# Kernel tuning notes

Hardware: AMD Instinct MI355X
Metric: run time of the kernel (lower is better)

## Reference

```python
import jax, jax.numpy as jnp
import numpy as np

N, NNODES, CIN, COUT = 64, 512, 32, 64


def setup_inputs() -> dict:
    key = jax.random.key(0)
    k1, k2, k3, k4, k5 = jax.random.split(key, 5)
    A = jax.random.normal(k1, (N, NNODES, NNODES), dtype=jnp.float32)
    X = jax.random.normal(k2, (N, NNODES, CIN), dtype=jnp.float32)
    A_coeffs = jax.random.normal(k3, (5 + 2 * CIN,), dtype=jnp.float32)
    x_num = 4 + 2 * CIN
    scale = np.sqrt(2.0) / (COUT + x_num)
    X_coeffs_1 = jax.random.normal(k4, (COUT, x_num), dtype=jnp.float32) * scale
    X_coeffs_2 = jax.random.normal(k5, (COUT, x_num), dtype=jnp.float32) * scale
    return {"A": A, "X": X, "A_coeffs": A_coeffs,
            "X_coeffs_1": X_coeffs_1, "X_coeffs_2": X_coeffs_2}


def _forward(A, X, A_coeffs, W1, W2):
    n = A.shape[-1]
    C = X.shape[-1]
    Xt = jnp.swapaxes(X, -1, -2)                      # N,C,n
    diag = jnp.diagonal(A, axis1=-2, axis2=-1)        # N,n
    mean_diag = diag.mean(-1)                         # N
    mean_cols = A.mean(-1)                            # N,n
    mean_all = mean_cols.mean(-1)                     # N
    mean_X = Xt.mean(-1)                              # N,C

    c = A_coeffs
    w6 = c[5:5 + C]                                   # coeffs for a6 (X_i + X_j)
    w7 = c[5 + C:5 + 2 * C]                           # coeffs for a7 (mean_X)
    # Fold the 'd,ndij->nij' contraction over the 7 basis tensors into
    # scalar/row/col broadcast terms (identical math, no N x (5+2C) x n x n tensor).
    s = jnp.einsum('c,nci->ni', w6, Xt)               # N,n
    const = c[1] * mean_all + c[2] * mean_diag + jnp.einsum('c,nc->n', w7, mean_X)
    vec = c[3] * mean_cols + c[4] * diag + s          # N,n
    A_t = c[0] * A + const[:, None, None] + vec[:, :, None] + vec[:, None, :]

    # X basis out_x: N x (4+2C) x n, order [x1, x2, x3, x4, x5, x6]
    ones_n = jnp.ones((1, 1, n), A.dtype)
    out_x = jnp.concatenate([
        Xt,                                           # x1: N,C,n
        mean_X[:, :, None] * ones_n,                  # x2: N,C,n
        mean_cols[:, None, :],                        # x3: N,1,n
        diag[:, None, :],                             # x4: N,1,n
        mean_diag[:, None, None] * ones_n,            # x5: N,1,n
        mean_all[:, None, None] * ones_n,             # x6: N,1,n
    ], axis=1)
    X1 = jnp.einsum('bd,ndi->nbi', W1, out_x)         # N,B,n
    X2 = jnp.einsum('bd,ndi->nbi', W2, out_x)         # N,B,n
    out = jnp.einsum('nij,nbj->nbi', A_t, X1) / n + X2  # N,B,n
    return jnp.swapaxes(out, -1, -2)                  # N,n,B


def reference(A, X, A_coeffs, X_coeffs_1, X_coeffs_2):
    return _forward(A, X, A_coeffs, X_coeffs_1, X_coeffs_2)
```

## Files before the change

kernel.cpp:

```cpp
#include <hip/hip_runtime.h>
#include <hip/hip_bf16.h>

#define NB 64
#define NN 512
#define CI 32
#define CO 64
#define XN 68
#define YR 80

typedef __attribute__((ext_vector_type(8))) short bf16x8;
typedef __attribute__((ext_vector_type(4))) float f32x4;

__device__ inline short f2bf(float f) {
  union { __hip_bfloat16 h; unsigned short u; } cv;
  cv.h = __float2bfloat16(f);
  return (short)cv.u;
}

__device__ inline bf16x8 cvt8(float4 a, float4 b) {
  bf16x8 r;
  r[0] = f2bf(a.x); r[1] = f2bf(a.y); r[2] = f2bf(a.z); r[3] = f2bf(a.w);
  r[4] = f2bf(b.x); r[5] = f2bf(b.y); r[6] = f2bf(b.z); r[7] = f2bf(b.w);
  return r;
}

__global__ __launch_bounds__(256) void k1x(
    const float* __restrict__ A, const float* __restrict__ X,
    const float* __restrict__ cf, const float* __restrict__ W1,
    float* __restrict__ mc, float* __restrict__ dg, float* __restrict__ vec,
    float* __restrict__ pA, float* __restrict__ pD,
    float* __restrict__ pmX, float* __restrict__ ptC, float* __restrict__ pS,
    unsigned short* __restrict__ Yext) {
  int b = blockIdx.x, ch = blockIdx.y;
  int t = threadIdx.x, w = t >> 6, lane = t & 63;
  int r0 = ch * 16;
  const float* Ab = A + (size_t)b * NN * NN;
  __shared__ float sXc[16][33];
  __shared__ float scf[69];
  __shared__ float sMc[16], sDg[16], sVec[16], wsum[4];

  if (t < 69) scf[t] = cf[t];
  {
    int j = t >> 4, c = (t & 15) * 2;
    float2 xv = *(const float2*)(X + ((size_t)b * NN + r0 + j) * CI + c);
    sXc[j][c] = xv.x; sXc[j][c + 1] = xv.y;
  }
  float4 v0[4], v1[4];
#pragma unroll
  for (int m = 0; m < 4; ++m) {
    const float* rp = Ab + (size_t)(r0 + w * 4 + m) * NN;
    v0[m] = *(const float4*)(rp + lane * 4);
    v1[m] = *(const float4*)(rp + 256 + lane * 4);
  }
  float accR = 0.f;
#pragma unroll
  for (int m = 0; m < 4; ++m) {
    float s = (v0[m].x + v0[m].y) + (v0[m].z + v0[m].w) +
              (v1[m].x + v1[m].y) + (v1[m].z + v1[m].w);
#pragma unroll
    for (int off = 1; off < 64; off <<= 1) s += __shfl_xor(s, off, 64);
    if (lane == 0) {
      float m_ = s * (1.0f / NN);
      mc[b * NN + r0 + w * 4 + m] = m_;
      sMc[w * 4 + m] = m_;
    }
    accR += s;
  }
  if (lane == 0) wsum[w] = accR;
  if (t < 16) {
    float d = Ab[(size_t)(r0 + t) * NN + r0 + t];
    dg[b * NN + r0 + t] = d;
    sDg[t] = d;
  }
  __syncthreads();

  float c0n = scf[0] * (1.0f / NN);

  if (t < 16) {
    float u = 0.f;
#pragma unroll
    for (int c = 0; c < CI; ++c) u += scf[5 + c] * sXc[t][c];
    float vj = scf[3] * sMc[t] + scf[4] * sDg[t] + u;
    vec[b * NN + r0 + t] = vj;
    sVec[t] = vj;
  } else if (t == 16) {
    pA[b * 32 + ch] = wsum[0] + wsum[1] + wsum[2] + wsum[3];
    float sd = 0.f;
#pragma unroll
    for (int k = 0; k < 16; ++k) sd += sDg[k];
    pD[b * 32 + ch] = sd;
  }

  {
    int ra = lane & 15, kg = lane >> 4, g = lane >> 4;
    const float* wp = W1 + (w * 16 + ra) * XN + kg * 8;
    bf16x8 wf = cvt8(*(const float4*)wp, *(const float4*)(wp + 4));
    const float* xp = &sXc[ra][kg * 8];
    bf16x8 xf = cvt8(*(const float4*)xp, *(const float4*)(xp + 4));
    f32x4 zero = {0.f, 0.f, 0.f, 0.f};
    f32x4 d = __builtin_amdgcn_mfma_f32_16x16x32_bf16(xf, wf, zero, 0, 0, 0);
    union { unsigned short u[4]; uint2 v; } pk;
#pragma unroll
    for (int r = 0; r < 4; ++r) pk.u[r] = (unsigned short)f2bf(d[r] * c0n);
    *(uint2*)(Yext + ((size_t)b * YR + w * 16 + ra) * NN + r0 + g * 4) = pk.v;
  }
  if (t < 16) {
    Yext[((size_t)b * YR + 64) * NN + r0 + t] = (unsigned short)f2bf(sMc[t] * c0n);
  } else if (t < 32) {
    Yext[((size_t)b * YR + 65) * NN + r0 + (t - 16)] = (unsigned short)f2bf(sDg[t - 16] * c0n);
  } else if (t < 32 + 224) {
    int u2 = t - 32;
    int row = 66 + (u2 >> 4), col = r0 + (u2 & 15);
    Yext[((size_t)b * YR + row) * NN + col] = 0;
  }
  __syncthreads();

  if (t < 32) {
    float s1 = 0.f, s2 = 0.f;
#pragma unroll
    for (int r = 0; r < 16; ++r) {
      float xv = sXc[r][t];
      s1 += xv;
      s2 += sVec[r] * xv;
    }
    pmX[((size_t)b * 32 + ch) * 32 + t] = s1;
    ptC[((size_t)b * 32 + ch) * 32 + t] = s2;
  } else if (t < 35) {
    float s = 0.f;
    if (t == 32) { for (int r = 0; r < 16; ++r) s += sVec[r]; }
    if (t == 33) { for (int r = 0; r < 16; ++r) s += sVec[r] * sMc[r]; }
    if (t == 34) { for (int r = 0; r < 16; ++r) s += sVec[r] * sDg[r]; }
    pS[((size_t)b * 32 + ch) * 3 + (t - 32)] = s;
  }
}

__global__ __launch_bounds__(256) void kW(
    const float* __restrict__ cf, const float* __restrict__ W1,
    const float* __restrict__ W2, const float* __restrict__ pA,
    const float* __restrict__ pD, const float* __restrict__ pmX,
    const float* __restrict__ ptC, const float* __restrict__ pS,
    float* __restrict__ colv, float* __restrict__ sconst) {
  int gb = blockIdx.x, t = threadIdx.x;
  int bb0 = gb * 4;
  __shared__ float sW1[64][69], sW2[64][69];
  __shared__ float mXs[4][33], tCs[4][33];
  __shared__ float scal[4][6];
  __shared__ float scf[69];
  if (t < 69) scf[t] = cf[t];
  for (int idx = t; idx < 64 * XN; idx += 256) {
    int r = idx / XN, c = idx - r * XN;
    sW1[r][c] = W1[idx];
    sW2[r][c] = W2[idx];
  }
  if (t < 128) {
    int bb = t >> 5, c = t & 31, b = bb0 + bb;
    float s1 = 0.f, s2 = 0.f;
#pragma unroll
    for (int k = 0; k < 32; ++k) {
      s1 += pmX[((size_t)b * 32 + k) * 32 + c];
      s2 += ptC[((size_t)b * 32 + k) * 32 + c];
    }
    mXs[bb][c] = s1 * (1.0f / NN);
    tCs[bb][c] = s2;
  } else if (t < 132) {
    int bb = t - 128, b = bb0 + bb;
    float sA = 0.f, sD = 0.f;
#pragma unroll
    for (int k = 0; k < 32; ++k) { sA += pA[b * 32 + k]; sD += pD[b * 32 + k]; }
    scal[bb][0] = sD * (1.0f / NN);
    scal[bb][1] = sA * (1.0f / ((float)NN * (float)NN));
  } else if (t < 136) {
    int bb = t - 132, b = bb0 + bb;
    float s1 = 0.f, s2 = 0.f, s3 = 0.f;
#pragma unroll
    for (int k = 0; k < 32; ++k) {
      s1 += pS[((size_t)b * 32 + k) * 3 + 0];
      s2 += pS[((size_t)b * 32 + k) * 3 + 1];
      s3 += pS[((size_t)b * 32 + k) * 3 + 2];
    }
    scal[bb][2] = s1; scal[bb][3] = s2; scal[bb][4] = s3;
  }
  __syncthreads();
  if (t < 4) {
    float s7 = 0.f;
#pragma unroll
    for (int c = 0; c < CI; ++c) s7 += scf[5 + CI + c] * mXs[t][c];
    sconst[bb0 + t] = scf[1] * scal[t][1] + scf[2] * scal[t][0] + s7;
  }
  {
    int bb = t >> 6, o = t & 63, b = bb0 + bb;
    float w1mX = 0.f, a1 = 0.f, a2 = 0.f, wt = 0.f;
#pragma unroll
    for (int c = 0; c < CI; ++c) {
      float m = mXs[bb][c];
      w1mX += sW1[o][c] * m;
      a1 += sW1[o][CI + c] * m;
      a2 += sW2[o][CI + c] * m;
      wt += sW1[o][c] * tCs[bb][c];
    }
    float smd = scal[bb][0], sma = scal[bb][1];
    a1 += sW1[o][66] * smd + sW1[o][67] * sma;
    a2 += sW2[o][66] * smd + sW2[o][67] * sma;
    float we0 = sW1[o][64], we1 = sW1[o][65];
    float S1n = w1mX + a1 + we0 * sma + we1 * smd;
    float SVn = (wt + a1 * scal[bb][2] + we0 * scal[bb][3] + we1 * scal[bb][4]) * (1.0f / NN);
    float4 cva = make_float4(S1n, a2 + SVn, sW2[o][64] + scf[0] * a1, sW2[o][65]);
    float4 cvb = make_float4(we0, we1, 0.f, 0.f);
    *(float4*)&colv[((size_t)b * CO + o) * 8] = cva;
    *(float4*)&colv[((size_t)b * CO + o) * 8 + 4] = cvb;
  }
}

__global__ __launch_bounds__(512, 4) void k5_mfma(
    const float* __restrict__ A, const unsigned short* __restrict__ Yext,
    const float* __restrict__ X, const float* __restrict__ W2,
    const float* __restrict__ vec, const float* __restrict__ mc,
    const float* __restrict__ dg, const float* __restrict__ colv,
    const float* __restrict__ sconst, float* __restrict__ out) {
  int ic = blockIdx.x, b = blockIdx.y;
  int t = threadIdx.x, w = t >> 6, lane = t & 63;
  int rg = w >> 1, oc = w & 1;
  int ra = lane & 15, kg = lane >> 4, g = lane >> 4;
  int i0 = ic * 64;
  int wr0 = rg * 16;
  __shared__ unsigned short sA[2][64 * 64];
  __shared__ float sGm[64], sGd[64];

  const unsigned short* Yb = Yext + (size_t)b * YR * NN;

  int st_r = t >> 3, st_k = t & 7;
  const float* Agl = A + ((size_t)(b * NN + i0 + st_r)) * NN + st_k * 8;
  int st_addr = st_r * 64 + ((st_k ^ (st_r & 7)) << 3);

  {
    float4 a0 = *(const float4*)(Agl);
    float4 a1 = *(const float4*)(Agl + 4);
    *(bf16x8*)&sA[0][st_addr] = cvt8(a0, a1);
  }
  __syncthreads();

  f32x4 acc[2] = {{0.f, 0.f, 0.f, 0.f}, {0.f, 0.f, 0.f, 0.f}};
  f32x4 acc4 = {0.f, 0.f, 0.f, 0.f};
  int arow = wr0 + ra;
  int abase = arow * 64;
  int aswz = arow & 7;

  for (int c = 0; c < 8; ++c) {
    int cur = c & 1;
    float4 na0, na1;
    if (c < 7) {
      na0 = *(const float4*)(Agl + (c + 1) * 64);
      na1 = *(const float4*)(Agl + (c + 1) * 64 + 4);
    }
#pragma unroll
    for (int kb = 0; kb < 2; ++kb) {
      bf16x8 af = *(const bf16x8*)&sA[cur][abase + (((kb * 4 + kg) ^ aswz) << 3)];
      int kcol = c * 64 + kb * 32 + kg * 8;
#pragma unroll
      for (int to = 0; to < 2; ++to) {
        bf16x8 bf = *(const bf16x8*)(Yb + (size_t)(oc * 32 + to * 16 + ra) * NN + kcol);
        acc[to] = __builtin_amdgcn_mfma_f32_16x16x32_bf16(af, bf, acc[to], 0, 0, 0);
      }
      if (oc == 0) {
        bf16x8 bf4 = *(const bf16x8*)(Yb + (size_t)(64 + ra) * NN + kcol);
        acc4 = __builtin_amdgcn_mfma_f32_16x16x32_bf16(af, bf4, acc4, 0, 0, 0);
      }
    }
    if (c < 7) {
      *(bf16x8*)&sA[cur ^ 1][st_addr] = cvt8(na0, na1);
    }
    __syncthreads();
  }

  {
    const float* xp = X + (size_t)(b * NN + i0 + wr0 + ra) * CI + kg * 8;
    bf16x8 xf = cvt8(*(const float4*)xp, *(const float4*)(xp + 4));
#pragma unroll
    for (int to = 0; to < 2; ++to) {
      const float* wp = W2 + (size_t)(oc * 32 + to * 16 + ra) * XN + kg * 8;
      bf16x8 wf = cvt8(*(const float4*)wp, *(const float4*)(wp + 4));
      acc[to] = __builtin_amdgcn_mfma_f32_16x16x32_bf16(xf, wf, acc[to], 0, 0, 0);
    }
  }

  if (oc == 0 && ra < 2) {
#pragma unroll
    for (int r = 0; r < 4; ++r) {
      if (ra == 0) sGm[wr0 + g * 4 + r] = acc4[r];
      else         sGd[wr0 + g * 4 + r] = acc4[r];
    }
  }
  __syncthreads();

  float4 v4 = *(const float4*)&vec[b * NN + i0 + wr0 + g * 4];
  float4 m4 = *(const float4*)&mc[b * NN + i0 + wr0 + g * 4];
  float4 d4 = *(const float4*)&dg[b * NN + i0 + wr0 + g * 4];
  float sc = sconst[b];
  float vp[4] = {v4.x + sc, v4.y + sc, v4.z + sc, v4.w + sc};
  float mr[4] = {m4.x, m4.y, m4.z, m4.w};
  float dr[4] = {d4.x, d4.y, d4.z, d4.w};
  float Gm[4], Gd[4];
#pragma unroll
  for (int r = 0; r < 4; ++r) {
    int row = wr0 + g * 4 + r;
    Gm[r] = sGm[row];
    Gd[r] = sGd[row];
  }

#pragma unroll
  for (int to = 0; to < 2; ++to) {
    int o = oc * 32 + to * 16 + ra;
    float4 cva = *(const float4*)&colv[((size_t)b * CO + o) * 8];
    float4 cvb = *(const float4*)&colv[((size_t)b * CO + o) * 8 + 4];
#pragma unroll
    for (int r = 0; r < 4; ++r) {
      float val = acc[to][r] + vp[r] * cva.x + cva.y + mr[r] * cva.z +
                  dr[r] * cva.w + Gm[r] * cvb.x + Gd[r] * cvb.y;
      out[((size_t)(b * NN + i0 + wr0 + g * 4 + r)) * CO + o] = val;
    }
  }
}

extern "C" void kernel_launch(void* const* d_in, const int* in_sizes, int n_in,
                              void* d_out, int out_size, void* d_ws, size_t ws_size,
                              hipStream_t stream) {
  const float* A = (const float*)d_in[0];
  const float* X = (const float*)d_in[1];
  const float* cf = (const float*)d_in[2];
  const float* W1 = (const float*)d_in[3];
  const float* W2 = (const float*)d_in[4];
  float* out = (float*)d_out;

  float* p = (float*)d_ws;
  float* mc = p;      p += NB * NN;
  float* dg = p;      p += NB * NN;
  float* vec = p;     p += NB * NN;
  float* pA = p;      p += NB * 32;
  float* pD = p;      p += NB * 32;
  float* pmX = p;     p += NB * 32 * 32;
  float* ptC = p;     p += NB * 32 * 32;
  float* pS = p;      p += NB * 32 * 3;
  float* colv = p;    p += NB * CO * 8;
  float* sconst = p;  p += NB;
  unsigned short* Yext = (unsigned short*)p;

  k1x<<<dim3(NB, 32), 256, 0, stream>>>(A, X, cf, W1, mc, dg, vec,
                                        pA, pD, pmX, ptC, pS, Yext);
  kW<<<16, 256, 0, stream>>>(cf, W1, W2, pA, pD, pmX, ptC, pS, colv, sconst);
  k5_mfma<<<dim3(8, NB), 512, 0, stream>>>(A, Yext, X, W2, vec, mc, dg,
                                           colv, sconst, out);
}
```

Baseline: 54.58 us.

## Block Y operand into k-tiled layout and halve k5 row tile

Stores the bf16 Y operand in a k-blocked layout (per batch, 16 k-blocks of 80 rows by 32 columns), so each MFMA B-fragment load reads from a compact contiguous tile instead of striding across 512-wide rows. The main GEMM kernel now processes 32 output rows per block with 256 threads, doubling the grid to 16x64 blocks. Smaller blocks may improve occupancy and load balance, but each A row tile's Y data is reread by twice as many blocks. Parts of k5 that are not shown, such as the epilogue using sGm and sGd, must match the new 32-row tile for this to be correct.

```diff
diff --git a/kernel.cpp b/kernel.cpp
--- a/kernel.cpp
+++ b/kernel.cpp
@@ -6,7 +6,6 @@
 #define CI 32
 #define CO 64
 #define XN 68
-#define YR 80
 
 typedef __attribute__((ext_vector_type(8))) short bf16x8;
 typedef __attribute__((ext_vector_type(4))) float f32x4;
@@ -30,10 +29,11 @@
     float* __restrict__ mc, float* __restrict__ dg, float* __restrict__ vec,
     float* __restrict__ pA, float* __restrict__ pD,
     float* __restrict__ pmX, float* __restrict__ ptC, float* __restrict__ pS,
-    unsigned short* __restrict__ Yext) {
+    unsigned short* __restrict__ Ybf) {
   int b = blockIdx.x, ch = blockIdx.y;
   int t = threadIdx.x, w = t >> 6, lane = t & 63;
   int r0 = ch * 16;
+  int kb = r0 >> 5, jbase = r0 & 16;
   const float* Ab = A + (size_t)b * NN * NN;
   __shared__ float sXc[16][33];
   __shared__ float scf[69];
@@ -102,16 +102,19 @@
     union { unsigned short u[4]; uint2 v; } pk;
 #pragma unroll
     for (int r = 0; r < 4; ++r) pk.u[r] = (unsigned short)f2bf(d[r] * c0n);
-    *(uint2*)(Yext + ((size_t)b * YR + w * 16 + ra) * NN + r0 + g * 4) = pk.v;
+    int o = w * 16 + ra;
+    *(uint2*)(Ybf + (((size_t)b * 16 + kb) * 80 + o) * 32 + jbase + g * 4) = pk.v;
   }
   if (t < 16) {
-    Yext[((size_t)b * YR + 64) * NN + r0 + t] = (unsigned short)f2bf(sMc[t] * c0n);
+    Ybf[(((size_t)b * 16 + kb) * 80 + 64) * 32 + jbase + t] =
+        (unsigned short)f2bf(sMc[t] * c0n);
   } else if (t < 32) {
-    Yext[((size_t)b * YR + 65) * NN + r0 + (t - 16)] = (unsigned short)f2bf(sDg[t - 16] * c0n);
+    Ybf[(((size_t)b * 16 + kb) * 80 + 65) * 32 + jbase + (t - 16)] =
+        (unsigned short)f2bf(sDg[t - 16] * c0n);
   } else if (t < 32 + 224) {
     int u2 = t - 32;
-    int row = 66 + (u2 >> 4), col = r0 + (u2 & 15);
-    Yext[((size_t)b * YR + row) * NN + col] = 0;
+    int row = 66 + (u2 >> 4), col = jbase + (u2 & 15);
+    Ybf[(((size_t)b * 16 + kb) * 80 + row) * 32 + col] = 0;
   }
   __syncthreads();
 
@@ -211,8 +214,8 @@
   }
 }
 
-__global__ __launch_bounds__(512, 4) void k5_mfma(
-    const float* __restrict__ A, const unsigned short* __restrict__ Yext,
+__global__ __launch_bounds__(256, 4) void k5_mfma(
+    const float* __restrict__ A, const unsigned short* __restrict__ Ybf,
     const float* __restrict__ X, const float* __restrict__ W2,
     const float* __restrict__ vec, const float* __restrict__ mc,
     const float* __restrict__ dg, const float* __restrict__ colv,
@@ -221,12 +224,12 @@
   int t = threadIdx.x, w = t >> 6, lane = t & 63;
   int rg = w >> 1, oc = w & 1;
   int ra = lane & 15, kg = lane >> 4, g = lane >> 4;
-  int i0 = ic * 64;
+  int i0 = ic * 32;
   int wr0 = rg * 16;
-  __shared__ unsigned short sA[2][64 * 64];
-  __shared__ float sGm[64], sGd[64];
-
-  const unsigned short* Yb = Yext + (size_t)b * YR * NN;
+  __shared__ unsigned short sA[2][32 * 64];
+  __shared__ float sGm[32], sGd[32];
+
+  const unsigned short* Yb = Ybf + (size_t)b * 16 * 80 * 32;
 
   int st_r = t >> 3, st_k = t & 7;
   const float* Agl = A + ((size_t)(b * NN + i0 + st_r)) * NN + st_k * 8;
@@ -253,16 +256,17 @@
       na1 = *(const float4*)(Agl + (c + 1) * 64 + 4);
     }
 #pragma unroll
-    for (int kb = 0; kb < 2; ++kb) {
-      bf16x8 af = *(const bf16x8*)&sA[cur][abase + (((kb * 4 + kg) ^ aswz) << 3)];
-      int kcol = c * 64 + kb * 32 + kg * 8;
+    for (int kbl = 0; kbl < 2; ++kbl) {
+      int kb = c * 2 + kbl;
+      bf16x8 af = *(const bf16x8*)&sA[cur][abase + (((kbl * 4 + kg) ^ aswz) << 3)];
+      const unsigned short* Ybb = Yb + ((size_t)kb * 80) * 32;
 #pragma unroll
       for (int to = 0; to < 2; ++to) {
-        bf16x8 bf = *(const bf16x8*)(Yb + (size_t)(oc * 32 + to * 16 + ra) * NN + kcol);
+        bf16x8 bf = *(const bf16x8*)(Ybb + (oc * 32 + to * 16 + ra) * 32 + kg * 8);
         acc[to] = __builtin_amdgcn_mfma_f32_16x16x32_bf16(af, bf, acc[to], 0, 0, 0);
       }
       if (oc == 0) {
-        bf16x8 bf4 = *(const bf16x8*)(Yb + (size_t)(64 + ra) * NN + kcol);
+        bf16x8 bf4 = *(const bf16x8*)(Ybb + (64 + ra) * 32 + kg * 8);
         acc4 = __builtin_amdgcn_mfma_f32_16x16x32_bf16(af, bf4, acc4, 0, 0, 0);
       }
     }
@@ -342,11 +346,11 @@
   float* pS = p;      p += NB * 32 * 3;
   float* colv = p;    p += NB * CO * 8;
   float* sconst = p;  p += NB;
-  unsigned short* Yext = (unsigned short*)p;
+  unsigned short* Ybf = (unsigned short*)p;
 
   k1x<<<dim3(NB, 32), 256, 0, stream>>>(A, X, cf, W1, mc, dg, vec,
-                                        pA, pD, pmX, ptC, pS, Yext);
+                                        pA, pD, pmX, ptC, pS, Ybf);
   kW<<<16, 256, 0, stream>>>(cf, W1, W2, pA, pD, pmX, ptC, pS, colv, sconst);
-  k5_mfma<<<dim3(8, NB), 512, 0, stream>>>(A, Yext, X, W2, vec, mc, dg,
-                                           colv, sconst, out);
-}
+  k5_mfma<<<dim3(16, NB), 256, 0, stream>>>(A, Ybf, X, W2, vec, mc, dg,
+                                            colv, sconst, out);
+}
```

Result: faster. 49.54 us (-9.2%).
